# Kernel optimization log

Hardware: AMD Instinct MI355X
Metric: run time of the kernel (lower is better)

## Reference

```python
import jax, jax.numpy as jnp
import numpy as np

# TT configuration (matches init_kwargs)
P = (100, 100, 100)      # tt_p_shapes, prod = num_embeddings = 1e6
Q = (4, 4, 8)            # tt_q_shapes, prod = embedding_dim = 128
R = (1, 32, 32, 1)       # tt_ranks padded with boundary 1s
D = 128                  # embedding_dim
B = 4096                 # batch size (number of bags)
H = 50                   # pooling factor (history length)
NNZ = B * H              # total indices


def setup_inputs() -> dict:
    key = jax.random.key(0)
    k1, k2, k3, k4 = jax.random.split(key, 4)
    # TT cores, stored flattened along trailing dims like TT-Rec:
    # core_i : [p_i, r_i * q_i * r_{i+1}]
    sigma = 0.1
    core0 = sigma * jax.random.normal(k1, (P[0], R[0] * Q[0] * R[1]), dtype=jnp.float32)
    core1 = sigma * jax.random.normal(k2, (P[1], R[1] * Q[1] * R[2]), dtype=jnp.float32)
    core2 = sigma * jax.random.normal(k3, (P[2], R[2] * Q[2] * R[3]), dtype=jnp.float32)
    indices = jax.random.randint(k4, (NNZ,), 0, P[0] * P[1] * P[2], dtype=jnp.int32)
    lengths = jnp.full((B,), H, dtype=jnp.int32)
    return {"indices": indices, "lengths": lengths,
            "core0": core0, "core1": core1, "core2": core2}


def reference(indices, lengths, core0, core1, core2):
    n = indices.shape[0]
    # mixed-radix decomposition of flat row index over p-shapes
    i1 = indices // (P[1] * P[2])
    i2 = (indices // P[2]) % P[1]
    i3 = indices % P[2]
    # gather per-index TT core slices
    a = core0[i1].reshape(n, Q[0], R[1])          # [n, q1, r1]
    b = core1[i2].reshape(n, R[1], Q[1], R[2])    # [n, r1, q2, r2]
    c = core2[i3].reshape(n, R[2], Q[2])          # [n, r2, q3]
    # TT contraction chain reconstructing each embedding row
    ab = jnp.einsum('nar,nrbs->nabs', a, b).reshape(n, Q[0] * Q[1], R[2])  # [n, q1*q2, r2]
    emb = jnp.einsum('nms,nsc->nmc', ab, c).reshape(n, D)                  # [n, D]
    # bag sum-pooling: rowidx = repeat_interleave(arange(B), lengths)
    batch = lengths.shape[0]
    rowidx = jnp.repeat(jnp.arange(batch, dtype=jnp.int32), lengths,
                        total_repeat_length=n)
    out = jax.ops.segment_sum(emb, rowidx, num_segments=batch)             # [B, D]
    return out
```

## Files before the change

kernel.cpp:

```cpp
#include <hip/hip_runtime.h>
#include <hip/hip_bf16.h>


#define P0 100
#define P1 100
#define P2 100
#define Q0 4
#define Q1 4
#define Q2 8
#define DIM 128
#define NPAIR (P0 * P1)

typedef __attribute__((ext_vector_type(8))) short short8v;
typedef __attribute__((ext_vector_type(4))) float f32x4;

__device__ inline short f2bf(float x) {
    union { __hip_bfloat16 h; short s; } u;
    u.h = __float2bfloat16(x);
    return u.s;
}

__global__ __launch_bounds__(256) void prep(const int* __restrict__ lengths, int B,
                                            const float* __restrict__ core0,
                                            const float* __restrict__ core1,
                                            const float* __restrict__ core2,
                                            int* __restrict__ offsets,
                                            __hip_bfloat16* __restrict__ bfrag,
                                            __hip_bfloat16* __restrict__ ab) {
    int bid = blockIdx.x;
    int t = threadIdx.x;
    if (bid == 0) {
        __shared__ int part[256];
        int per = (B + 255) / 256;
        int s = 0;
        for (int k = 0; k < per; ++k) {
            int i = t * per + k;
            s += (i < B) ? lengths[i] : 0;
        }
        part[t] = s;
        __syncthreads();
        for (int d = 1; d < 256; d <<= 1) {
            int v = (t >= d) ? part[t - d] : 0;
            __syncthreads();
            part[t] += v;
            __syncthreads();
        }
        int run = part[t] - s;
        for (int k = 0; k < per; ++k) {
            int i = t * per + k;
            if (i < B) { offsets[i] = run; run += lengths[i]; }
        }
        if (t == 255) offsets[B] = part[255];
    } else if (bid <= P2) {
        if (t < 64 && !(t & 8)) {
            int i3 = bid - 1;
            int h = t >> 4, c3 = t & 7;
            const float* crow = core2 + (size_t)i3 * (32 * Q2);
            __hip_bfloat16* o = bfrag + (size_t)i3 * 256 + h * 64 + c3 * 8;
#pragma unroll
            for (int j = 0; j < 8; ++j)
                o[j] = __float2bfloat16(crow[(h * 8 + j) * Q2 + c3]);
        }
    } else {
        int g = bid - 1 - P2;
        int i2 = g >> 1;
        int w = t >> 6, lane = t & 63;
        int ct = (g & 1) * 4 + w;
        int h = lane >> 4;
        int c16 = lane & 15;

        const float* bbase = core1 + (size_t)i2 * 4096 + (h * 8) * 128 + ct * 16 + c16;
        short8v bfr;
#pragma unroll
        for (int j = 0; j < 8; ++j) bfr[j] = f2bf(bbase[j * 128]);

        int col = ct * 16 + c16;
        for (int rt = 0; rt < 25; ++rt) {
            const float* abase = core0 + (size_t)(rt * 4 + (c16 >> 2)) * 128
                                 + (c16 & 3) * 32 + h * 8;
            f32x4 x0 = *(const f32x4*)abase;
            f32x4 x1 = *(const f32x4*)(abase + 4);
            short8v afr;
#pragma unroll
            for (int j = 0; j < 4; ++j) { afr[j] = f2bf(x0[j]); afr[j + 4] = f2bf(x1[j]); }

            f32x4 d = __builtin_amdgcn_mfma_f32_16x16x32_bf16(
                afr, bfr, (f32x4){0.f, 0.f, 0.f, 0.f}, 0, 0, 0);

            __hip_bfloat16* dst = ab + (size_t)((rt * 4 + h) * P1 + i2) * 512
                                  + (col >> 5) * 32 + (col & 31);
#pragma unroll
            for (int q = 0; q < 4; ++q) dst[q * 128] = __float2bfloat16(d[q]);
        }
    }
}

__global__ __launch_bounds__(256, 6) void bag_pool(const int* __restrict__ indices, int n,
                                                   const int* __restrict__ offsets, int B,
                                                   const char* __restrict__ ab,
                                                   const char* __restrict__ bfrag,
                                                   float* __restrict__ out) {
    int w = threadIdx.x >> 6;
    int lane = threadIdx.x & 63;
    int bag = blockIdx.x * 2 + (w >> 1);
    int half = w & 1;

    int start = 0, end = 0;
    if (bag < B) {
        start = offsets[bag];
        end = offsets[bag + 1];
        if (bag == B - 1 && end < n) end = n;
        if (end > n) end = n;
        if (start > n) start = n;
        if (end < start) end = start;
    }
    int cnt = end - start;
    int c0 = (cnt + 1) >> 1;
    int mystart = start + (half ? c0 : 0);
    int mycnt = half ? (cnt - c0) : c0;

    int aoff = (lane & 15) * 64 + (lane >> 4) * 16;
    int boff = (lane >> 4) * 128 + (lane & 7) * 16;

    f32x4 acc0 = {0.f, 0.f, 0.f, 0.f};
    f32x4 acc1 = {0.f, 0.f, 0.f, 0.f};
    f32x4 acc2 = {0.f, 0.f, 0.f, 0.f};
    f32x4 acc3 = {0.f, 0.f, 0.f, 0.f};

    for (int cb = 0; cb < mycnt; cb += 64) {
        int m = mycnt - cb;
        if (m > 64) m = 64;
        unsigned idx = 0;
        if (lane < m) idx = (unsigned)indices[mystart + cb + lane];
        unsigned p = idx / 100u;
        unsigned i3 = idx - p * 100u;
        int abo = (int)(p << 10);
        int bfo = (int)(i3 << 9);

        int j = 0;
        for (; j + 3 < m; j += 4) {
            int A0 = __shfl(abo, j),     B0 = __shfl(bfo, j);
            int A1 = __shfl(abo, j + 1), B1 = __shfl(bfo, j + 1);
            int A2 = __shfl(abo, j + 2), B2 = __shfl(bfo, j + 2);
            int A3 = __shfl(abo, j + 3), B3 = __shfl(bfo, j + 3);
            short8v a0 = *(const short8v*)(ab + A0 + aoff);
            short8v b0 = *(const short8v*)(bfrag + B0 + boff);
            short8v a1 = *(const short8v*)(ab + A1 + aoff);
            short8v b1 = *(const short8v*)(bfrag + B1 + boff);
            short8v a2 = *(const short8v*)(ab + A2 + aoff);
            short8v b2 = *(const short8v*)(bfrag + B2 + boff);
            short8v a3 = *(const short8v*)(ab + A3 + aoff);
            short8v b3 = *(const short8v*)(bfrag + B3 + boff);
            acc0 = __builtin_amdgcn_mfma_f32_16x16x32_bf16(a0, b0, acc0, 0, 0, 0);
            acc1 = __builtin_amdgcn_mfma_f32_16x16x32_bf16(a1, b1, acc1, 0, 0, 0);
            acc2 = __builtin_amdgcn_mfma_f32_16x16x32_bf16(a2, b2, acc2, 0, 0, 0);
            acc3 = __builtin_amdgcn_mfma_f32_16x16x32_bf16(a3, b3, acc3, 0, 0, 0);
        }
        for (; j < m; ++j) {
            int A0 = __shfl(abo, j), B0 = __shfl(bfo, j);
            short8v a0 = *(const short8v*)(ab + A0 + aoff);
            short8v b0 = *(const short8v*)(bfrag + B0 + boff);
            acc0 = __builtin_amdgcn_mfma_f32_16x16x32_bf16(a0, b0, acc0, 0, 0, 0);
        }
    }
    f32x4 acc = (acc0 + acc1) + (acc2 + acc3);

    __shared__ f32x4 red[2][64];
    if (half) red[w >> 1][lane] = acc;
    __syncthreads();
    if (!half) {
        acc += red[w >> 1][lane];
        int col = lane & 15;
        if (bag < B && col < 8) {
            int rb = (lane >> 4) * 4;
            float* orow = out + (size_t)bag * DIM;
#pragma unroll
            for (int q = 0; q < 4; ++q)
                orow[(rb + q) * 8 + col] = acc[q];
        }
    }
}

__global__ __launch_bounds__(128) void fallback_pool(const int* __restrict__ indices,
                                                     int n, int B,
                                                     const float* __restrict__ core0,
                                                     const float* __restrict__ core1,
                                                     const float* __restrict__ core2,
                                                     float* __restrict__ out) {
    int bag = blockIdx.x;
    int d = threadIdx.x;
    int m = d >> 3, c3 = d & 7;
    int a_ = m >> 2, b_ = m & 3;
    int H = n / B;
    float acc = 0.f;
    for (int j = bag * H; j < (bag + 1) * H; ++j) {
        int idx = indices[j];
        int i1 = idx / (P1 * P2);
        int rem = idx - i1 * (P1 * P2);
        int i2 = rem / P2;
        int i3 = rem - i2 * P2;
        const float* a = core0 + (size_t)i1 * 128;
        const float* b = core1 + (size_t)i2 * 4096;
        const float* c = core2 + (size_t)i3 * 256;
        float e = 0.f;
        for (int s = 0; s < 32; ++s) {
            float abv = 0.f;
            for (int r = 0; r < 32; ++r)
                abv += a[a_ * 32 + r] * b[r * 128 + b_ * 32 + s];
            e += abv * c[s * 8 + c3];
        }
        acc += e;
    }
    out[(size_t)bag * DIM + d] = acc;
}

extern "C" void kernel_launch(void* const* d_in, const int* in_sizes, int n_in,
                              void* d_out, int out_size, void* d_ws, size_t ws_size,
                              hipStream_t stream) {
    const int* indices = (const int*)d_in[0];
    const int* lengths = (const int*)d_in[1];
    const float* core0 = (const float*)d_in[2];
    const float* core1 = (const float*)d_in[3];
    const float* core2 = (const float*)d_in[4];
    float* out = (float*)d_out;
    int n = in_sizes[0];
    int B = in_sizes[1];

    const size_t OFF_OFFSETS = 0;
    const size_t OFF_BFRAG = 32768;
    const size_t OFF_AB = 131072;
    const size_t REQ = OFF_AB + (size_t)NPAIR * 1024;

    if (ws_size >= REQ) {
        int* offsets = (int*)((char*)d_ws + OFF_OFFSETS);
        __hip_bfloat16* bfragp = (__hip_bfloat16*)((char*)d_ws + OFF_BFRAG);
        __hip_bfloat16* abt = (__hip_bfloat16*)((char*)d_ws + OFF_AB);

        prep<<<1 + P2 + 200, 256, 0, stream>>>(lengths, B, core0, core1, core2,
                                               offsets, bfragp, abt);
        bag_pool<<<(B + 1) / 2, 256, 0, stream>>>(indices, n, offsets, B,
                                                  (const char*)abt, (const char*)bfragp, out);
    } else {
        fallback_pool<<<B, 128, 0, stream>>>(indices, n, B, core0, core1, core2, out);
    }
}
```

Measured before the change: 43.29 us.

## Split AB table into two halves mapped to XCD groups with atomic pooling

Splits the precomputed bf16 AB table into two half-tables along the output row dimension. Blocks are assigned so that each XCD group reads only one half, which shrinks the working set per L2 cache. Each wave now handles a full bag for one half and packs two indices per MFMA using the two 8-lane groups, with a padded zero B-fragment for odd tails. Output is combined with atomicAdd after a memset, replacing the shared-memory reduction. This adds an extra memset launch and atomic traffic, and the speedup depends on the blockIdx-to-XCD round-robin mapping assumption.

```diff
diff --git a/kernel.cpp b/kernel.cpp
--- a/kernel.cpp
+++ b/kernel.cpp
@@ -5,11 +5,10 @@
 #define P0 100
 #define P1 100
 #define P2 100
-#define Q0 4
-#define Q1 4
 #define Q2 8
 #define DIM 128
 #define NPAIR (P0 * P1)
+#define NULL_BFO (P2 * 512)
 
 typedef __attribute__((ext_vector_type(8))) short short8v;
 typedef __attribute__((ext_vector_type(4))) float f32x4;
@@ -26,10 +25,12 @@
                                             const float* __restrict__ core2,
                                             int* __restrict__ offsets,
                                             __hip_bfloat16* __restrict__ bfrag,
-                                            __hip_bfloat16* __restrict__ ab) {
+                                            __hip_bfloat16* __restrict__ ab0,
+                                            __hip_bfloat16* __restrict__ ab1) {
     int bid = blockIdx.x;
     int t = threadIdx.x;
     if (bid == 0) {
+        ((short*)bfrag)[P2 * 256 + t] = 0;
         __shared__ int part[256];
         int per = (B + 255) / 256;
         int s = 0;
@@ -75,6 +76,8 @@
         for (int j = 0; j < 8; ++j) bfr[j] = f2bf(bbase[j * 128]);
 
         int col = ct * 16 + c16;
+        int cs = col >> 5;
+        int s = col & 31;
         for (int rt = 0; rt < 25; ++rt) {
             const float* abase = core0 + (size_t)(rt * 4 + (c16 >> 2)) * 128
                                  + (c16 & 3) * 32 + h * 8;
@@ -87,55 +90,57 @@
             f32x4 d = __builtin_amdgcn_mfma_f32_16x16x32_bf16(
                 afr, bfr, (f32x4){0.f, 0.f, 0.f, 0.f}, 0, 0, 0);
 
-            __hip_bfloat16* dst = ab + (size_t)((rt * 4 + h) * P1 + i2) * 512
-                                  + (col >> 5) * 32 + (col & 31);
-#pragma unroll
-            for (int q = 0; q < 4; ++q) dst[q * 128] = __float2bfloat16(d[q]);
-        }
-    }
-}
-
-__global__ __launch_bounds__(256, 6) void bag_pool(const int* __restrict__ indices, int n,
-                                                   const int* __restrict__ offsets, int B,
-                                                   const char* __restrict__ ab,
-                                                   const char* __restrict__ bfrag,
-                                                   float* __restrict__ out) {
+            int pair = (rt * 4 + h) * P1 + i2;
+#pragma unroll
+            for (int q = 0; q < 4; ++q) {
+                int m = q * 4 + cs;
+                __hip_bfloat16* tbl = (m & 8) ? ab1 : ab0;
+                tbl[(size_t)pair * 256 + (m & 7) * 32 + s] = __float2bfloat16(d[q]);
+            }
+        }
+    }
+}
+
+__global__ __launch_bounds__(256) void bag_pool(const int* __restrict__ indices, int n,
+                                                const int* __restrict__ offsets, int B,
+                                                const char* __restrict__ ab0,
+                                                const char* __restrict__ ab1,
+                                                const char* __restrict__ bfrag,
+                                                float* __restrict__ out) {
     int w = threadIdx.x >> 6;
     int lane = threadIdx.x & 63;
-    int bag = blockIdx.x * 2 + (w >> 1);
-    int half = w & 1;
-
-    int start = 0, end = 0;
-    if (bag < B) {
-        start = offsets[bag];
-        end = offsets[bag + 1];
-        if (bag == B - 1 && end < n) end = n;
-        if (end > n) end = n;
-        if (start > n) start = n;
-        if (end < start) end = start;
-    }
+    int g = blockIdx.x >> 3;
+    int xcd = blockIdx.x & 7;
+    int half = xcd >> 2;
+    int bag = (g * 4 + (xcd & 3)) * 4 + w;
+    if (bag >= B) return;
+
+    const char* tbl = half ? ab1 : ab0;
+
+    int start = offsets[bag];
+    int end = offsets[bag + 1];
+    if (bag == B - 1 && end < n) end = n;
+    if (end > n) end = n;
+    if (start > n) start = n;
+    if (end < start) end = start;
     int cnt = end - start;
-    int c0 = (cnt + 1) >> 1;
-    int mystart = start + (half ? c0 : 0);
-    int mycnt = half ? (cnt - c0) : c0;
-
-    int aoff = (lane & 15) * 64 + (lane >> 4) * 16;
+
+    int sel = (lane >> 3) & 1;
+    int aoff = (lane & 7) * 64 + (lane >> 4) * 16;
     int boff = (lane >> 4) * 128 + (lane & 7) * 16;
 
     f32x4 acc0 = {0.f, 0.f, 0.f, 0.f};
     f32x4 acc1 = {0.f, 0.f, 0.f, 0.f};
-    f32x4 acc2 = {0.f, 0.f, 0.f, 0.f};
-    f32x4 acc3 = {0.f, 0.f, 0.f, 0.f};
-
-    for (int cb = 0; cb < mycnt; cb += 64) {
-        int m = mycnt - cb;
+
+    for (int cb = 0; cb < cnt; cb += 64) {
+        int m = cnt - cb;
         if (m > 64) m = 64;
         unsigned idx = 0;
-        if (lane < m) idx = (unsigned)indices[mystart + cb + lane];
+        if (lane < m) idx = (unsigned)indices[start + cb + lane];
         unsigned p = idx / 100u;
         unsigned i3 = idx - p * 100u;
-        int abo = (int)(p << 10);
-        int bfo = (int)(i3 << 9);
+        int abo = (int)(p << 9);
+        int bfo = (lane < m) ? (int)(i3 << 9) : NULL_BFO;
 
         int j = 0;
         for (; j + 3 < m; j += 4) {
@@ -143,40 +148,38 @@
             int A1 = __shfl(abo, j + 1), B1 = __shfl(bfo, j + 1);
             int A2 = __shfl(abo, j + 2), B2 = __shfl(bfo, j + 2);
             int A3 = __shfl(abo, j + 3), B3 = __shfl(bfo, j + 3);
-            short8v a0 = *(const short8v*)(ab + A0 + aoff);
-            short8v b0 = *(const short8v*)(bfrag + B0 + boff);
-            short8v a1 = *(const short8v*)(ab + A1 + aoff);
-            short8v b1 = *(const short8v*)(bfrag + B1 + boff);
-            short8v a2 = *(const short8v*)(ab + A2 + aoff);
-            short8v b2 = *(const short8v*)(bfrag + B2 + boff);
-            short8v a3 = *(const short8v*)(ab + A3 + aoff);
-            short8v b3 = *(const short8v*)(bfrag + B3 + boff);
+            int Ae = sel ? A1 : A0, Be = sel ? B1 : B0;
+            int Af = sel ? A3 : A2, Bf = sel ? B3 : B2;
+            short8v a0 = *(const short8v*)(tbl + Ae + aoff);
+            short8v b0 = *(const short8v*)(bfrag + Be + boff);
+            short8v a1 = *(const short8v*)(tbl + Af + aoff);
+            short8v b1 = *(const short8v*)(bfrag + Bf + boff);
             acc0 = __builtin_amdgcn_mfma_f32_16x16x32_bf16(a0, b0, acc0, 0, 0, 0);
             acc1 = __builtin_amdgcn_mfma_f32_16x16x32_bf16(a1, b1, acc1, 0, 0, 0);
-            acc2 = __builtin_amdgcn_mfma_f32_16x16x32_bf16(a2, b2, acc2, 0, 0, 0);
-            acc3 = __builtin_amdgcn_mfma_f32_16x16x32_bf16(a3, b3, acc3, 0, 0, 0);
-        }
-        for (; j < m; ++j) {
-            int A0 = __shfl(abo, j), B0 = __shfl(bfo, j);
-            short8v a0 = *(const short8v*)(ab + A0 + aoff);
-            short8v b0 = *(const short8v*)(bfrag + B0 + boff);
+        }
+        for (; j < m; j += 2) {
+            int A0 = __shfl(abo, j),     B0 = __shfl(bfo, j);
+            int A1 = __shfl(abo, j + 1), B1 = __shfl(bfo, j + 1);
+            int Ae = sel ? A1 : A0, Be = sel ? B1 : B0;
+            short8v a0 = *(const short8v*)(tbl + Ae + aoff);
+            short8v b0 = *(const short8v*)(bfrag + Be + boff);
             acc0 = __builtin_amdgcn_mfma_f32_16x16x32_bf16(a0, b0, acc0, 0, 0, 0);
         }
     }
-    f32x4 acc = (acc0 + acc1) + (acc2 + acc3);
-
-    __shared__ f32x4 red[2][64];
-    if (half) red[w >> 1][lane] = acc;
-    __syncthreads();
-    if (!half) {
-        acc += red[w >> 1][lane];
-        int col = lane & 15;
-        if (bag < B && col < 8) {
-            int rb = (lane >> 4) * 4;
-            float* orow = out + (size_t)bag * DIM;
-#pragma unroll
-            for (int q = 0; q < 4; ++q)
-                orow[(rb + q) * 8 + col] = acc[q];
+    f32x4 acc = acc0 + acc1;
+
+#pragma unroll
+    for (int q = 0; q < 4; ++q) {
+        float o = __shfl(acc[q], (lane + 40) & 63);
+        acc[q] += o;
+    }
+    int hi = lane >> 4, c3 = lane & 15;
+    if (hi < 2 && c3 < 8) {
+        float* obase = out + (size_t)bag * DIM;
+#pragma unroll
+        for (int q = 0; q < 4; ++q) {
+            int d = (half * 8 + hi * 4 + q) * 8 + c3;
+            atomicAdd(obase + d, acc[q]);
         }
     }
 }
@@ -228,18 +231,23 @@
 
     const size_t OFF_OFFSETS = 0;
     const size_t OFF_BFRAG = 32768;
-    const size_t OFF_AB = 131072;
-    const size_t REQ = OFF_AB + (size_t)NPAIR * 1024;
+    const size_t OFF_AB0 = 131072;
+    const size_t OFF_AB1 = OFF_AB0 + (size_t)NPAIR * 512;
+    const size_t REQ = OFF_AB1 + (size_t)NPAIR * 512;
 
     if (ws_size >= REQ) {
         int* offsets = (int*)((char*)d_ws + OFF_OFFSETS);
         __hip_bfloat16* bfragp = (__hip_bfloat16*)((char*)d_ws + OFF_BFRAG);
-        __hip_bfloat16* abt = (__hip_bfloat16*)((char*)d_ws + OFF_AB);
-
+        __hip_bfloat16* abt0 = (__hip_bfloat16*)((char*)d_ws + OFF_AB0);
+        __hip_bfloat16* abt1 = (__hip_bfloat16*)((char*)d_ws + OFF_AB1);
+
+        hipMemsetAsync(d_out, 0, (size_t)out_size * sizeof(float), stream);
         prep<<<1 + P2 + 200, 256, 0, stream>>>(lengths, B, core0, core1, core2,
-                                               offsets, bfragp, abt);
-        bag_pool<<<(B + 1) / 2, 256, 0, stream>>>(indices, n, offsets, B,
-                                                  (const char*)abt, (const char*)bfragp, out);
+                                               offsets, bfragp, abt0, abt1);
+        int grid = ((B + 15) / 16) * 8;
+        bag_pool<<<grid, 256, 0, stream>>>(indices, n, offsets, B,
+                                           (const char*)abt0, (const char*)abt1,
+                                           (const char*)bfragp, out);
     } else {
         fallback_pool<<<B, 128, 0, stream>>>(indices, n, B, core0, core1, core2, out);
     }
```

New measurement: 46.98 us. 1.09x slower.

## Stage AB products through LDS for coalesced stores and prefetch core0 in prep

Applied to the files above, without the earlier changes.

The prep kernel now runs 512-thread blocks. Each block computes all 8 column tiles for one i2 but only half of the row tiles. MFMA results are staged in shared memory so that each pair row is written as a coalesced 8-byte vector store, replacing scattered 2-byte stores. Core0 loads are software-prefetched one iteration ahead, and the core2 fragment conversion is folded into block 0 to remove 100 tiny blocks. In exchange, the kernel adds a __syncthreads per row tile and serialises the bfrag work onto the scan block.

```diff
diff --git a/kernel.cpp b/kernel.cpp
--- a/kernel.cpp
+++ b/kernel.cpp
@@ -12,6 +12,7 @@
 #define NPAIR (P0 * P1)
 
 typedef __attribute__((ext_vector_type(8))) short short8v;
+typedef __attribute__((ext_vector_type(4))) short short4v;
 typedef __attribute__((ext_vector_type(4))) float f32x4;
 
 __device__ inline short f2bf(float x) {
@@ -20,18 +21,20 @@
     return u.s;
 }
 
-__global__ __launch_bounds__(256) void prep(const int* __restrict__ lengths, int B,
+__global__ __launch_bounds__(512) void prep(const int* __restrict__ lengths, int B,
                                             const float* __restrict__ core0,
                                             const float* __restrict__ core1,
                                             const float* __restrict__ core2,
                                             int* __restrict__ offsets,
                                             __hip_bfloat16* __restrict__ bfrag,
                                             __hip_bfloat16* __restrict__ ab) {
+    __shared__ int part[512];
+    __shared__ short lds_ab[2048];
     int bid = blockIdx.x;
     int t = threadIdx.x;
+
     if (bid == 0) {
-        __shared__ int part[256];
-        int per = (B + 255) / 256;
+        int per = (B + 511) / 512;
         int s = 0;
         for (int k = 0; k < per; ++k) {
             int i = t * per + k;
@@ -39,7 +42,7 @@
         }
         part[t] = s;
         __syncthreads();
-        for (int d = 1; d < 256; d <<= 1) {
+        for (int d = 1; d < 512; d <<= 1) {
             int v = (t >= d) ? part[t - d] : 0;
             __syncthreads();
             part[t] += v;
@@ -50,22 +53,20 @@
             int i = t * per + k;
             if (i < B) { offsets[i] = run; run += lengths[i]; }
         }
-        if (t == 255) offsets[B] = part[255];
-    } else if (bid <= P2) {
-        if (t < 64 && !(t & 8)) {
-            int i3 = bid - 1;
-            int h = t >> 4, c3 = t & 7;
-            const float* crow = core2 + (size_t)i3 * (32 * Q2);
-            __hip_bfloat16* o = bfrag + (size_t)i3 * 256 + h * 64 + c3 * 8;
-#pragma unroll
-            for (int j = 0; j < 8; ++j)
-                o[j] = __float2bfloat16(crow[(h * 8 + j) * Q2 + c3]);
+        if (t == 511) offsets[B] = part[511];
+
+        for (int e = t; e < P2 * 256; e += 512) {
+            int i3 = e >> 8, r = e & 255;
+            int hq = r >> 6, c3 = (r >> 3) & 7, j = r & 7;
+            bfrag[e] = __float2bfloat16(core2[(size_t)i3 * 256 + (hq * 8 + j) * Q2 + c3]);
         }
     } else {
-        int g = bid - 1 - P2;
+        int g = bid - 1;
         int i2 = g >> 1;
+        int rtbase = (g & 1) * 13;
+        int nrt = (g & 1) ? 12 : 13;
         int w = t >> 6, lane = t & 63;
-        int ct = (g & 1) * 4 + w;
+        int ct = w;
         int h = lane >> 4;
         int c16 = lane & 15;
 
@@ -75,11 +76,23 @@
         for (int j = 0; j < 8; ++j) bfr[j] = f2bf(bbase[j * 128]);
 
         int col = ct * 16 + c16;
-        for (int rt = 0; rt < 25; ++rt) {
-            const float* abase = core0 + (size_t)(rt * 4 + (c16 >> 2)) * 128
-                                 + (c16 & 3) * 32 + h * 8;
-            f32x4 x0 = *(const f32x4*)abase;
-            f32x4 x1 = *(const f32x4*)(abase + 4);
+        int cs = col >> 5;
+        int sl = col & 31;
+        const short* lsrc = lds_ab + (t >> 7) * 512 + (t & 127) * 4;
+        short* ab_s = (short*)ab;
+
+        const float* abase0 = core0 + (size_t)(c16 >> 2) * 128 + (c16 & 3) * 32 + h * 8;
+
+        f32x4 x0 = *(const f32x4*)(abase0 + (size_t)rtbase * 512);
+        f32x4 x1 = *(const f32x4*)(abase0 + (size_t)rtbase * 512 + 4);
+        for (int k = 0; k < nrt; ++k) {
+            int rtg = rtbase + k;
+            if (k) __syncthreads();
+            f32x4 y0, y1;
+            if (k + 1 < nrt) {
+                y0 = *(const f32x4*)(abase0 + (size_t)(rtg + 1) * 512);
+                y1 = *(const f32x4*)(abase0 + (size_t)(rtg + 1) * 512 + 4);
+            }
             short8v afr;
 #pragma unroll
             for (int j = 0; j < 4; ++j) { afr[j] = f2bf(x0[j]); afr[j + 4] = f2bf(x1[j]); }
@@ -87,10 +100,16 @@
             f32x4 d = __builtin_amdgcn_mfma_f32_16x16x32_bf16(
                 afr, bfr, (f32x4){0.f, 0.f, 0.f, 0.f}, 0, 0, 0);
 
-            __hip_bfloat16* dst = ab + (size_t)((rt * 4 + h) * P1 + i2) * 512
-                                  + (col >> 5) * 32 + (col & 31);
-#pragma unroll
-            for (int q = 0; q < 4; ++q) dst[q * 128] = __float2bfloat16(d[q]);
+#pragma unroll
+            for (int q = 0; q < 4; ++q)
+                lds_ab[h * 512 + (q * 4 + cs) * 32 + sl] = f2bf(d[q]);
+            __syncthreads();
+
+            int pair = (rtg * 4 + (t >> 7)) * P1 + i2;
+            *(short4v*)(ab_s + (size_t)pair * 512 + (t & 127) * 4) =
+                *(const short4v*)lsrc;
+
+            x0 = y0; x1 = y1;
         }
     }
 }
@@ -236,8 +255,8 @@
         __hip_bfloat16* bfragp = (__hip_bfloat16*)((char*)d_ws + OFF_BFRAG);
         __hip_bfloat16* abt = (__hip_bfloat16*)((char*)d_ws + OFF_AB);
 
-        prep<<<1 + P2 + 200, 256, 0, stream>>>(lengths, B, core0, core1, core2,
-                                               offsets, bfragp, abt);
+        prep<<<1 + 200, 512, 0, stream>>>(lengths, B, core0, core1, core2,
+                                          offsets, bfragp, abt);
         bag_pool<<<(B + 1) / 2, 256, 0, stream>>>(indices, n, offsets, B,
                                                   (const char*)abt, (const char*)bfragp, out);
     } else {
```

Result: slower. 46.03 us (+6.3%).

## Fuse prep and bag pooling into one cooperative kernel with grid sync

Applied to the files above, without the earlier changes.

Merges the prep stage (core0×core1 product table, core2 fragment repack, offset scan) and the bag pooling into a single cooperative kernel launched with 1024 blocks, separated by a grid-wide sync. The product-table build now does two MFMA column tiles per wave, prefetches the next core0 slice, and stages results in LDS so the global writes are wide and coalesced. The aim is to remove the second launch and the inter-kernel gap. In exchange, pooling blocks loop over bags in a grid-stride fashion with fewer resident blocks, and the grid sync adds a cost. The small-workspace fallback kernel is dropped.

```diff
diff --git a/kernel.cpp b/kernel.cpp
--- a/kernel.cpp
+++ b/kernel.cpp
@@ -1,12 +1,13 @@
 #include <hip/hip_runtime.h>
 #include <hip/hip_bf16.h>
+#include <hip/hip_cooperative_groups.h>
+
+namespace cg = cooperative_groups;
 
 
 #define P0 100
 #define P1 100
 #define P2 100
-#define Q0 4
-#define Q1 4
 #define Q2 8
 #define DIM 128
 #define NPAIR (P0 * P1)
@@ -18,6 +19,194 @@
     union { __hip_bfloat16 h; short s; } u;
     u.h = __float2bfloat16(x);
     return u.s;
+}
+
+__global__ __launch_bounds__(256, 4) void fused(const int* __restrict__ indices,
+                                                const int* __restrict__ lengths,
+                                                const float* __restrict__ core0,
+                                                const float* __restrict__ core1,
+                                                const float* __restrict__ core2,
+                                                int n, int B,
+                                                int* __restrict__ offsets,
+                                                __hip_bfloat16* __restrict__ bfrag,
+                                                __hip_bfloat16* __restrict__ ab,
+                                                float* __restrict__ out) {
+    __shared__ int part[256];
+    __shared__ short lds_ab[2048];
+    __shared__ f32x4 red[2][64];
+
+    int bid = blockIdx.x;
+    int t = threadIdx.x;
+
+    if (bid < 200) {
+        int i2 = bid >> 1;
+        int rtbase = (bid & 1) * 13;
+        int nrt = (bid & 1) ? 12 : 13;
+        int w = t >> 6, lane = t & 63;
+        int h = lane >> 4;
+        int c16 = lane & 15;
+
+        const float* bb0 = core1 + (size_t)i2 * 4096 + (h * 8) * 128 + w * 16 + c16;
+        short8v bfr0, bfr1;
+#pragma unroll
+        for (int j = 0; j < 8; ++j) {
+            bfr0[j] = f2bf(bb0[j * 128]);
+            bfr1[j] = f2bf(bb0[j * 128 + 64]);
+        }
+        int col0 = w * 16 + c16;
+        int cs0 = col0 >> 5;
+        int sl = col0 & 31;
+
+        const float* abase0 = core0 + (size_t)(c16 >> 2) * 128 + (c16 & 3) * 32 + h * 8;
+        const short* lsrc = lds_ab + (t >> 6) * 512 + (t & 63) * 8;
+        short* ab_s = (short*)ab;
+
+        f32x4 x0 = *(const f32x4*)(abase0 + (size_t)rtbase * 512);
+        f32x4 x1 = *(const f32x4*)(abase0 + (size_t)rtbase * 512 + 4);
+        for (int k = 0; k < nrt; ++k) {
+            int rtg = rtbase + k;
+            if (k) __syncthreads();
+            f32x4 y0, y1;
+            if (k + 1 < nrt) {
+                y0 = *(const f32x4*)(abase0 + (size_t)(rtg + 1) * 512);
+                y1 = *(const f32x4*)(abase0 + (size_t)(rtg + 1) * 512 + 4);
+            }
+            short8v afr;
+#pragma unroll
+            for (int j = 0; j < 4; ++j) { afr[j] = f2bf(x0[j]); afr[j + 4] = f2bf(x1[j]); }
+
+            f32x4 d0 = __builtin_amdgcn_mfma_f32_16x16x32_bf16(
+                afr, bfr0, (f32x4){0.f, 0.f, 0.f, 0.f}, 0, 0, 0);
+            f32x4 d1 = __builtin_amdgcn_mfma_f32_16x16x32_bf16(
+                afr, bfr1, (f32x4){0.f, 0.f, 0.f, 0.f}, 0, 0, 0);
+
+#pragma unroll
+            for (int q = 0; q < 4; ++q) {
+                lds_ab[h * 512 + (q * 4 + cs0) * 32 + sl] = f2bf(d0[q]);
+                lds_ab[h * 512 + (q * 4 + cs0 + 2) * 32 + sl] = f2bf(d1[q]);
+            }
+            __syncthreads();
+
+            int pair = (rtg * 4 + (t >> 6)) * P1 + i2;
+            *(short8v*)(ab_s + (size_t)pair * 512 + (t & 63) * 8) =
+                *(const short8v*)lsrc;
+
+            x0 = y0; x1 = y1;
+        }
+    } else if (bid < 300) {
+        int e = (bid - 200) * 256 + t;
+        int i3 = e >> 8, r = e & 255;
+        int hq = r >> 6, c3 = (r >> 3) & 7, j = r & 7;
+        bfrag[e] = __float2bfloat16(core2[(size_t)i3 * 256 + (hq * 8 + j) * Q2 + c3]);
+    } else if (bid == 300) {
+        int per = (B + 255) / 256;
+        int s = 0;
+        for (int k = 0; k < per; ++k) {
+            int i = t * per + k;
+            s += (i < B) ? lengths[i] : 0;
+        }
+        part[t] = s;
+        __syncthreads();
+        for (int d = 1; d < 256; d <<= 1) {
+            int v = (t >= d) ? part[t - d] : 0;
+            __syncthreads();
+            part[t] += v;
+            __syncthreads();
+        }
+        int run = part[t] - s;
+        for (int k = 0; k < per; ++k) {
+            int i = t * per + k;
+            if (i < B) { offsets[i] = run; run += lengths[i]; }
+        }
+        if (t == 255) offsets[B] = part[255];
+    }
+
+    cg::this_grid().sync();
+
+    const char* abc = (const char*)ab;
+    const char* bfc = (const char*)bfrag;
+    int w = t >> 6;
+    int lane = t & 63;
+    int nblk2 = (B + 1) / 2;
+    for (int blk = bid; blk < nblk2; blk += gridDim.x) {
+        int bag = blk * 2 + (w >> 1);
+        int half = w & 1;
+
+        int start = 0, end = 0;
+        if (bag < B) {
+            start = offsets[bag];
+            end = offsets[bag + 1];
+            if (bag == B - 1 && end < n) end = n;
+            if (end > n) end = n;
+            if (start > n) start = n;
+            if (end < start) end = start;
+        }
+        int cnt = end - start;
+        int c0 = (cnt + 1) >> 1;
+        int mystart = start + (half ? c0 : 0);
+        int mycnt = half ? (cnt - c0) : c0;
+
+        int aoff = (lane & 15) * 64 + (lane >> 4) * 16;
+        int boff = (lane >> 4) * 128 + (lane & 7) * 16;
+
+        f32x4 acc0 = {0.f, 0.f, 0.f, 0.f};
+        f32x4 acc1 = {0.f, 0.f, 0.f, 0.f};
+        f32x4 acc2 = {0.f, 0.f, 0.f, 0.f};
+        f32x4 acc3 = {0.f, 0.f, 0.f, 0.f};
+
+        for (int cb = 0; cb < mycnt; cb += 64) {
+            int m = mycnt - cb;
+            if (m > 64) m = 64;
+            unsigned idx = 0;
+            if (lane < m) idx = (unsigned)indices[mystart + cb + lane];
+            unsigned p = idx / 100u;
+            unsigned i3 = idx - p * 100u;
+            int abo = (int)(p << 10);
+            int bfo = (int)(i3 << 9);
+
+            int j = 0;
+            for (; j + 3 < m; j += 4) {
+                int A0 = __shfl(abo, j),     B0 = __shfl(bfo, j);
+                int A1 = __shfl(abo, j + 1), B1 = __shfl(bfo, j + 1);
+                int A2 = __shfl(abo, j + 2), B2 = __shfl(bfo, j + 2);
+                int A3 = __shfl(abo, j + 3), B3 = __shfl(bfo, j + 3);
+                short8v a0 = *(const short8v*)(abc + A0 + aoff);
+                short8v b0 = *(const short8v*)(bfc + B0 + boff);
+                short8v a1 = *(const short8v*)(abc + A1 + aoff);
+                short8v b1 = *(const short8v*)(bfc + B1 + boff);
+                short8v a2 = *(const short8v*)(abc + A2 + aoff);
+                short8v b2 = *(const short8v*)(bfc + B2 + boff);
+                short8v a3 = *(const short8v*)(abc + A3 + aoff);
+                short8v b3 = *(const short8v*)(bfc + B3 + boff);
+                acc0 = __builtin_amdgcn_mfma_f32_16x16x32_bf16(a0, b0, acc0, 0, 0, 0);
+                acc1 = __builtin_amdgcn_mfma_f32_16x16x32_bf16(a1, b1, acc1, 0, 0, 0);
+                acc2 = __builtin_amdgcn_mfma_f32_16x16x32_bf16(a2, b2, acc2, 0, 0, 0);
+                acc3 = __builtin_amdgcn_mfma_f32_16x16x32_bf16(a3, b3, acc3, 0, 0, 0);
+            }
+            for (; j < m; ++j) {
+                int A0 = __shfl(abo, j), B0 = __shfl(bfo, j);
+                short8v a0 = *(const short8v*)(abc + A0 + aoff);
+                short8v b0 = *(const short8v*)(bfc + B0 + boff);
+                acc0 = __builtin_amdgcn_mfma_f32_16x16x32_bf16(a0, b0, acc0, 0, 0, 0);
+            }
+        }
+        f32x4 acc = (acc0 + acc1) + (acc2 + acc3);
+
+        if (half) red[w >> 1][lane] = acc;
+        __syncthreads();
+        if (!half) {
+            acc += red[w >> 1][lane];
+            int col = lane & 15;
+            if (bag < B && col < 8) {
+                int rb = (lane >> 4) * 4;
+                float* orow = out + (size_t)bag * DIM;
+#pragma unroll
+                for (int q = 0; q < 4; ++q)
+                    orow[(rb + q) * 8 + col] = acc[q];
+            }
+        }
+        __syncthreads();
+    }
 }
 
 __global__ __launch_bounds__(256) void prep(const int* __restrict__ lengths, int B,
@@ -68,12 +257,10 @@
         int ct = (g & 1) * 4 + w;
         int h = lane >> 4;
         int c16 = lane & 15;
-
         const float* bbase = core1 + (size_t)i2 * 4096 + (h * 8) * 128 + ct * 16 + c16;
         short8v bfr;
 #pragma unroll
         for (int j = 0; j < 8; ++j) bfr[j] = f2bf(bbase[j * 128]);
-
         int col = ct * 16 + c16;
         for (int rt = 0; rt < 25; ++rt) {
             const float* abase = core0 + (size_t)(rt * 4 + (c16 >> 2)) * 128
@@ -83,10 +270,8 @@
             short8v afr;
 #pragma unroll
             for (int j = 0; j < 4; ++j) { afr[j] = f2bf(x0[j]); afr[j + 4] = f2bf(x1[j]); }
-
             f32x4 d = __builtin_amdgcn_mfma_f32_16x16x32_bf16(
                 afr, bfr, (f32x4){0.f, 0.f, 0.f, 0.f}, 0, 0, 0);
-
             __hip_bfloat16* dst = ab + (size_t)((rt * 4 + h) * P1 + i2) * 512
                                   + (col >> 5) * 32 + (col & 31);
 #pragma unroll
@@ -104,7 +289,6 @@
     int lane = threadIdx.x & 63;
     int bag = blockIdx.x * 2 + (w >> 1);
     int half = w & 1;
-
     int start = 0, end = 0;
     if (bag < B) {
         start = offsets[bag];
@@ -118,15 +302,12 @@
     int c0 = (cnt + 1) >> 1;
     int mystart = start + (half ? c0 : 0);
     int mycnt = half ? (cnt - c0) : c0;
-
     int aoff = (lane & 15) * 64 + (lane >> 4) * 16;
     int boff = (lane >> 4) * 128 + (lane & 7) * 16;
-
     f32x4 acc0 = {0.f, 0.f, 0.f, 0.f};
     f32x4 acc1 = {0.f, 0.f, 0.f, 0.f};
     f32x4 acc2 = {0.f, 0.f, 0.f, 0.f};
     f32x4 acc3 = {0.f, 0.f, 0.f, 0.f};
-
     for (int cb = 0; cb < mycnt; cb += 64) {
         int m = mycnt - cb;
         if (m > 64) m = 64;
@@ -136,7 +317,6 @@
         unsigned i3 = idx - p * 100u;
         int abo = (int)(p << 10);
         int bfo = (int)(i3 << 9);
-
         int j = 0;
         for (; j + 3 < m; j += 4) {
             int A0 = __shfl(abo, j),     B0 = __shfl(bfo, j);
@@ -164,7 +344,6 @@
         }
     }
     f32x4 acc = (acc0 + acc1) + (acc2 + acc3);
-
     __shared__ f32x4 red[2][64];
     if (half) red[w >> 1][lane] = acc;
     __syncthreads();
@@ -179,39 +358,6 @@
                 orow[(rb + q) * 8 + col] = acc[q];
         }
     }
-}
-
-__global__ __launch_bounds__(128) void fallback_pool(const int* __restrict__ indices,
-                                                     int n, int B,
-                                                     const float* __restrict__ core0,
-                                                     const float* __restrict__ core1,
-                                                     const float* __restrict__ core2,
-                                                     float* __restrict__ out) {
-    int bag = blockIdx.x;
-    int d = threadIdx.x;
-    int m = d >> 3, c3 = d & 7;
-    int a_ = m >> 2, b_ = m & 3;
-    int H = n / B;
-    float acc = 0.f;
-    for (int j = bag * H; j < (bag + 1) * H; ++j) {
-        int idx = indices[j];
-        int i1 = idx / (P1 * P2);
-        int rem = idx - i1 * (P1 * P2);
-        int i2 = rem / P2;
-        int i3 = rem - i2 * P2;
-        const float* a = core0 + (size_t)i1 * 128;
-        const float* b = core1 + (size_t)i2 * 4096;
-        const float* c = core2 + (size_t)i3 * 256;
-        float e = 0.f;
-        for (int s = 0; s < 32; ++s) {
-            float abv = 0.f;
-            for (int r = 0; r < 32; ++r)
-                abv += a[a_ * 32 + r] * b[r * 128 + b_ * 32 + s];
-            e += abv * c[s * 8 + c3];
-        }
-        acc += e;
-    }
-    out[(size_t)bag * DIM + d] = acc;
 }
 
 extern "C" void kernel_launch(void* const* d_in, const int* in_sizes, int n_in,
@@ -231,16 +377,25 @@
     const size_t OFF_AB = 131072;
     const size_t REQ = OFF_AB + (size_t)NPAIR * 1024;
 
-    if (ws_size >= REQ) {
-        int* offsets = (int*)((char*)d_ws + OFF_OFFSETS);
-        __hip_bfloat16* bfragp = (__hip_bfloat16*)((char*)d_ws + OFF_BFRAG);
-        __hip_bfloat16* abt = (__hip_bfloat16*)((char*)d_ws + OFF_AB);
-
+    if (ws_size < REQ) {
+    }
+
+    int* offsets = (int*)((char*)d_ws + OFF_OFFSETS);
+    __hip_bfloat16* bfragp = (__hip_bfloat16*)((char*)d_ws + OFF_BFRAG);
+    __hip_bfloat16* abt = (__hip_bfloat16*)((char*)d_ws + OFF_AB);
+
+    void* args[] = {
+        (void*)&indices, (void*)&lengths, (void*)&core0, (void*)&core1,
+        (void*)&core2, (void*)&n, (void*)&B, (void*)&offsets,
+        (void*)&bfragp, (void*)&abt, (void*)&out
+    };
+    hipError_t err = hipLaunchCooperativeKernel((const void*)fused, dim3(1024),
+                                                dim3(256), args, 0, stream);
+    if (err != hipSuccess) {
         prep<<<1 + P2 + 200, 256, 0, stream>>>(lengths, B, core0, core1, core2,
                                                offsets, bfragp, abt);
         bag_pool<<<(B + 1) / 2, 256, 0, stream>>>(indices, n, offsets, B,
-                                                  (const char*)abt, (const char*)bfragp, out);
-    } else {
-        fallback_pool<<<B, 128, 0, stream>>>(indices, n, B, core0, core1, core2, out);
+                                                  (const char*)abt, (const char*)bfragp,
+                                                  out);
     }
 }
```

After: 171.1 us. 295% more time.
